# Optimization experiments

Measured on AMD Instinct MI355X. Metric: run time of the kernel, lower is better.

Reference implementation:

```python
import jax, jax.numpy as jnp
import numpy as np

B = 8       # complexes in batch
C = 32      # CDR residues per antibody
G = 2048    # antigen nodes per complex
D = 128     # encoded_dims
N_AB = B * C
N_AG = B * G
N = N_AB + N_AG
SLOPE = 0.2
EPS_BN = 1e-5


def _build_edges():
    # block-sparse bipartite edges (cdr_b x ag_b), symmetrized, + self loops
    srcs, dsts = [], []
    for b in range(B):
        ab = np.arange(b * C, (b + 1) * C)
        ag = np.arange(N_AB + b * G, N_AB + (b + 1) * G)
        g1, g2 = np.meshgrid(ab, ag, indexing='ij')
        srcs.append(g1.ravel()); dsts.append(g2.ravel())
    s = np.concatenate(srcs); d = np.concatenate(dsts)
    loops = np.arange(N)
    src = np.concatenate([s, d, loops]).astype(np.int32)
    dst = np.concatenate([d, s, loops]).astype(np.int32)
    return src, dst


def setup_inputs() -> dict:
    key = jax.random.key(0)
    ks = jax.random.split(key, 16)
    sc = 1.0 / np.sqrt(D)
    edge_src, edge_dst = _build_edges()
    return {
        'selected_ab': jax.random.normal(ks[0], (N_AB, D), jnp.float32),
        'x_ag': jax.random.normal(ks[1], (N_AG, D), jnp.float32),
        'W1': jax.random.normal(ks[2], (D, D), jnp.float32) * sc,
        'a_src1': jax.random.normal(ks[3], (D,), jnp.float32) * sc,
        'a_dst1': jax.random.normal(ks[4], (D,), jnp.float32) * sc,
        'b1': jnp.zeros((D,), jnp.float32),
        'W2': jax.random.normal(ks[5], (D, D), jnp.float32) * sc,
        'a_src2': jax.random.normal(ks[6], (D,), jnp.float32) * sc,
        'a_dst2': jax.random.normal(ks[7], (D,), jnp.float32) * sc,
        'b2': jnp.zeros((D,), jnp.float32),
        'bn_ab_g': jnp.ones((2 * D,), jnp.float32),
        'bn_ab_b': jnp.zeros((2 * D,), jnp.float32),
        'bn_ag_g': jnp.ones((2 * D,), jnp.float32),
        'bn_ag_b': jnp.zeros((2 * D,), jnp.float32),
        'fc_w': jax.random.normal(ks[8], (2 * D, 1), jnp.float32) * sc,
        'fc_b': jnp.zeros((1,), jnp.float32),
        'agfc_w': jax.random.normal(ks[9], (2 * D, 1), jnp.float32) * sc,
        'agfc_b': jnp.zeros((1,), jnp.float32),
        'edge_src': jnp.asarray(edge_src),
        'edge_dst': jnp.asarray(edge_dst),
    }


def _gat(x, W, a_s, a_d, b, src, dst):
    # PyG GATConv, heads=1, eval mode (dropout off)
    h = x @ W                                  # [N, D]
    al_s = h @ a_s                             # [N]
    al_d = h @ a_d                             # [N]
    e = jax.nn.leaky_relu(al_s[src] + al_d[dst], SLOPE)   # [E]
    m = jax.ops.segment_max(e, dst, num_segments=N)
    e = jnp.exp(e - m[dst])
    z = jax.ops.segment_sum(e, dst, num_segments=N)
    alpha = e / (z[dst] + 1e-16)
    out = jax.ops.segment_sum(h[src] * alpha[:, None], dst, num_segments=N)
    return out + b


def _bn(x, g, b):
    # training-mode batch stats (biased variance), like torch BatchNorm1d
    m = x.mean(0)
    v = ((x - m) ** 2).mean(0)
    return (x - m) / jnp.sqrt(v + EPS_BN) * g + b


def reference(selected_ab, x_ag, W1, a_src1, a_dst1, b1, W2, a_src2, a_dst2, b2,
              bn_ab_g, bn_ab_b, bn_ag_g, bn_ag_b, fc_w, fc_b, agfc_w, agfc_b,
              edge_src, edge_dst):
    x = jnp.concatenate([selected_ab, x_ag], axis=0)          # [N, D]
    x = jax.nn.relu(_gat(x, W1, a_src1, a_dst1, b1, edge_src, edge_dst))
    x = _gat(x, W2, a_src2, a_dst2, b2, edge_src, edge_dst)
    x_ab = jnp.concatenate([x[:N_AB], selected_ab], axis=1)   # [N_ab, 2D]
    x_ab = jax.nn.relu(_bn(x_ab, bn_ab_g, bn_ab_b))
    x_ab = (x_ab @ fc_w + fc_b).ravel()
    x_ag_o = jnp.concatenate([x[N_AB:], x_ag], axis=1)        # [N_ag, 2D]
    x_ag_o = jax.nn.relu(_bn(x_ag_o, bn_ag_g, bn_ag_b))
    x_ag_o = (x_ag_o @ agfc_w + agfc_b).ravel()
    return (x_ab, x_ag_o)
```

## Files before the change

kernel.cpp:

```cpp
#include <hip/hip_runtime.h>


#define N_AB 256
#define N_AG 16384
#define N_ALL 16640
#define G_AG 2048
#define SLOPE 0.2f
#define MSHIFT 20.0f

typedef __attribute__((ext_vector_type(4))) float f32x4;
typedef __attribute__((ext_vector_type(8))) __bf16 bf16x8;
typedef __attribute__((ext_vector_type(8))) unsigned short u16x8;
typedef unsigned short ushort_t;

__device__ __forceinline__ float bf2f(ushort_t u) {
  union { unsigned int i; float f; } v; v.i = ((unsigned int)u) << 16; return v.f;
}
__device__ __forceinline__ ushort_t f2bf(float f) {
  union { float fv; unsigned int i; } v; v.fv = f;
  unsigned int x = v.i;
  return (ushort_t)((x + 0x7fffu + ((x >> 16) & 1u)) >> 16);
}
__device__ __forceinline__ float lrelu(float x) { return x >= 0.f ? x : SLOPE * x; }
__device__ __forceinline__ float expw(float e) {
  return __expf(fminf(e, 60.f) - MSHIFT);
}
__device__ __forceinline__ float ldf(const void* p, size_t i, int f) {
  return f ? ((const float*)p)[i] : bf2f(((const ushort_t*)p)[i]);
}
__device__ __forceinline__ void ld8f(const void* p, size_t i, int f, float* o) {
  if (f) {
    const f32x4* q = (const f32x4*)((const float*)p + i);
    f32x4 a = q[0], b = q[1];
#pragma unroll
    for (int j = 0; j < 4; ++j) { o[j] = a[j]; o[j + 4] = b[j]; }
  } else {
    u16x8 v = *(const u16x8*)((const ushort_t*)p + i);
#pragma unroll
    for (int j = 0; j < 8; ++j) o[j] = bf2f(v[j]);
  }
}

__global__ __launch_bounds__(256) void k_pre(
    const void* __restrict__ W1, const void* __restrict__ W2,
    const void* __restrict__ as1, const void* __restrict__ ad1,
    const void* __restrict__ as2, const void* __restrict__ ad2,
    const ushort_t* __restrict__ selu,
    ushort_t* __restrict__ W1t, ushort_t* __restrict__ W2t,
    float* __restrict__ va, float* __restrict__ bnsumAG,
    float* __restrict__ accf, float* __restrict__ accz,
    int* __restrict__ flagp) {
  int t = threadIdx.x, lane = t & 63, wid = t >> 6;
  int bx = blockIdx.x;
  int cnt = 0;
#pragma unroll
  for (int i = 0; i < 8; ++i) {
    unsigned e = (selu[lane * 8 + i] >> 7) & 0xFF;
    if (e > 0xC8) cnt++;
  }
  int f = (__popcll(__ballot(cnt > 0)) >= 3) ? 1 : 0;
  if (bx == 0 && t == 0) flagp[0] = f;

  if (bx < 16) {
    const void* W = (bx < 8) ? W1 : W2;
    ushort_t* Wt = (bx < 8) ? W1t : W2t;
    int base = (bx & 7) * 2048 + t * 8;
    float o[8];
    ld8f(W, base, f, o);
#pragma unroll
    for (int j = 0; j < 8; ++j) {
      int idx = base + j;
      Wt[(idx & 127) * 128 + (idx >> 7)] = f2bf(o[j]);
    }
  } else if (bx < 32) {
    int j = bx - 16;
    const void* W   = (j < 8) ? W1 : W2;
    const void* asv = (j < 8) ? as1 : as2;
    const void* adv = (j < 8) ? ad1 : ad2;
    int vbase = (j < 8) ? 0 : 256;
    int basek = (j & 7) * 16 + wid * 4;
    float a_s0 = ldf(asv, lane, f), a_s1 = ldf(asv, lane + 64, f);
    float a_d0 = ldf(adv, lane, f), a_d1 = ldf(adv, lane + 64, f);
#pragma unroll
    for (int i = 0; i < 4; ++i) {
      int k = basek + i;
      float w0 = ldf(W, (size_t)k * 128 + lane, f);
      float w1 = ldf(W, (size_t)k * 128 + lane + 64, f);
      float ps = w0 * a_s0 + w1 * a_s1;
      float pd = w0 * a_d0 + w1 * a_d1;
#pragma unroll
      for (int o = 1; o < 64; o <<= 1) {
        ps += __shfl_xor(ps, o);
        pd += __shfl_xor(pd, o);
      }
      if (lane == 0) { va[vbase + k] = ps; va[vbase + 128 + k] = pd; }
    }
  } else {
    int j = bx - 32;
    f32x4* az = (f32x4*)(accf + (size_t)j * 4096);
    f32x4 z4 = (f32x4){0.f, 0.f, 0.f, 0.f};
    for (int i = t; i < 1024; i += 256) az[i] = z4;
    if (j == 0) { bnsumAG[t] = 0.f; bnsumAG[t + 256] = 0.f; accz[t] = 0.f; }
  }
}

__global__ __launch_bounds__(256) void k_gemm(
    const void* __restrict__ xa, int modeA,
    const void* __restrict__ xb, int modeB,
    const int* __restrict__ flagp,
    const ushort_t* __restrict__ Wt, const float* __restrict__ va,
    ushort_t* __restrict__ h, float* __restrict__ als, float* __restrict__ ald,
    float* __restrict__ accf, float* __restrict__ accz,
    const void* __restrict__ biasAb, float* __restrict__ xabf, int do_abfin) {
  __shared__ float zsh[32], wsh[32];
  int t = threadIdx.x, lane = t & 63, wid = t >> 6;
  int bx = blockIdx.x;
  if (do_abfin && bx < 8) {
    int fr = *flagp;
    int b = bx;
    if (t < 32) {
      int grow = b * 32 + t;
      float w = expw(lrelu(als[grow] + ald[grow]));
      zsh[t] = accz[grow] + w;
      wsh[t] = w;
      accz[grow] = 0.f;
    }
    __syncthreads();
#pragma unroll
    for (int i = 0; i < 16; ++i) {
      int e = i * 256 + t;
      int rl = e >> 7, col = e & 127;
      int grow = b * 32 + rl;
      size_t idx = (size_t)grow * 128 + col;
      float hv = bf2f(h[idx]);
      float v = (accf[idx] + wsh[rl] * hv) / (zsh[rl] + 1e-16f) + ldf(biasAb, col, fr);
      accf[idx] = 0.f;
      v = fmaxf(v, 0.f);
      xabf[idx] = v;
    }
    __syncthreads();
  }

  int rw0 = bx * 32 + (wid >> 1) * 16;
  int ch = wid & 1;
  const void* xsrc; int roff, mode;
  if (rw0 < N_AB) { xsrc = xa; roff = rw0; mode = modeA; }
  else            { xsrc = xb; roff = rw0 - N_AB; mode = modeB; }
  int fx = (mode == 2) ? *flagp : mode;
  int mm = lane & 15, q = lane >> 4;
  f32x4 acc[4];
#pragma unroll
  for (int b = 0; b < 4; ++b) acc[b] = (f32x4){0.f, 0.f, 0.f, 0.f};
  float pals = 0.f, pald = 0.f;
#pragma unroll
  for (int s = 0; s < 4; ++s) {
    int koff = s * 32 + q * 8;
    union { u16x8 u; bf16x8 b; } af;
    float o[8];
    ld8f(xsrc, (size_t)(roff + mm) * 128 + koff, fx, o);
#pragma unroll
    for (int j = 0; j < 8; ++j) {
      af.u[j] = f2bf(o[j]);
      pals += o[j] * va[koff + j];
      pald += o[j] * va[128 + koff + j];
    }
#pragma unroll
    for (int nt = 0; nt < 4; ++nt) {
      int colb = ch * 64 + nt * 16;
      bf16x8 bfr = *(const bf16x8*)(Wt + (size_t)(colb + mm) * 128 + koff);
      acc[nt] = __builtin_amdgcn_mfma_f32_16x16x32_bf16(af.b, bfr, acc[nt], 0, 0, 0);
    }
  }
  if (ch == 0) {
    float s1 = pals; s1 += __shfl_xor(s1, 16); s1 += __shfl_xor(s1, 32);
    float d1 = pald; d1 += __shfl_xor(d1, 16); d1 += __shfl_xor(d1, 32);
    if (lane < 16) { als[rw0 + lane] = s1; ald[rw0 + lane] = d1; }
  }
#pragma unroll
  for (int nt = 0; nt < 4; ++nt)
#pragma unroll
    for (int r = 0; r < 4; ++r) {
      int row = rw0 + q * 4 + r;
      int col = ch * 64 + nt * 16 + mm;
      h[(size_t)row * 128 + col] = f2bf(acc[nt][r]);
    }
}

#define ABP_STRIDE 72
#define AG_STRIDE 40
__global__ __launch_bounds__(256) void k_agg(
    const ushort_t* __restrict__ h, const float* __restrict__ als,
    const float* __restrict__ ald, const void* __restrict__ bias,
    const int* __restrict__ flagp, ushort_t* __restrict__ xout,
    float* __restrict__ accf, float* __restrict__ accz,
    const void* __restrict__ x_ag, float* __restrict__ bnsumAG,
    int do_relu, int do_bnsum) {
  __shared__ ushort_t hT[128 * ABP_STRIDE];
  __shared__ float alsS[64];
  __shared__ float colsum[128], colsq[128];
  int bx = blockIdx.x;
  int t = threadIdx.x, lane = t & 63, wid = t >> 6;
  int mm = lane & 15, q = lane >> 4;

  if (bx < 256) {
    int b = bx >> 5, jt = bx & 31;
    int f = *flagp;
    {
      int row = t & 31, c0g = (t >> 5) * 16;
      const ushort_t* src = h + (size_t)(b * 32 + row) * 128 + c0g;
      u16x8 v0 = *(const u16x8*)src;
      u16x8 v1 = *(const u16x8*)(src + 8);
#pragma unroll
      for (int j = 0; j < 8; ++j) {
        hT[(c0g + j) * AG_STRIDE + row] = v0[j];
        hT[(c0g + 8 + j) * AG_STRIDE + row] = v1[j];
      }
      if (t < 32) alsS[t] = als[b * 32 + t];
      if (t < 128) { colsum[t] = 0.f; colsq[t] = 0.f; }
    }
    __syncthreads();
    int jl = jt * 64 + wid * 16;
    int jrow = N_AB + b * G_AG + jl;
    float aldj = ald[jrow + mm];
    float alsj = als[jrow + mm];
    union { u16x8 u; bf16x8 b; } af;
    float zp = 0.f;
#pragma unroll
    for (int j = 0; j < 8; ++j) {
      ushort_t us = f2bf(expw(lrelu(alsS[q * 8 + j] + aldj)));
      af.u[j] = us;
      zp += bf2f(us);
    }
    zp += __shfl_xor(zp, 16);
    zp += __shfl_xor(zp, 32);
    float wself = expw(lrelu(alsj + aldj));
    float z = zp + wself;
#pragma unroll
    for (int nt = 0; nt < 8; ++nt) {
      int col = nt * 16 + mm;
      union { u16x8 u; bf16x8 b; } bfr;
      bfr.b = *(const bf16x8*)(&hT[col * AG_STRIDE + q * 8]);
      f32x4 acc = {0.f, 0.f, 0.f, 0.f};
      acc = __builtin_amdgcn_mfma_f32_16x16x32_bf16(af.b, bfr.b, acc, 0, 0, 0);
      float biasv = ldf(bias, col, f);
      float sl = 0.f, sq = 0.f;
#pragma unroll
      for (int r = 0; r < 4; ++r) {
        int row = q * 4 + r;
        float zr = __shfl(z, row);
        float wsr = __shfl(wself, row);
        float hv = bf2f(h[(size_t)(jrow + row) * 128 + col]);
        float v = (acc[r] + wsr * hv) / (zr + 1e-16f) + biasv;
        sl += v; sq += v * v;
        if (do_relu) v = fmaxf(v, 0.f);
        xout[(size_t)(jrow + row) * 128 + col] = f2bf(v);
      }
      if (do_bnsum) {
        atomicAdd(&colsum[col], sl);
        atomicAdd(&colsq[col], sq);
      }
    }
    if (do_bnsum) {
      __syncthreads();
      if (t < 128) {
        atomicAdd(&bnsumAG[t], colsum[t]);
        atomicAdd(&bnsumAG[256 + t], colsq[t]);
      }
    }
  } else if (bx < 512) {
    int bx2 = bx - 256;
    int b = bx2 >> 5, sg = bx2 & 31;
    int jrow0 = N_AB + b * G_AG + sg * 64;
    {
      int jr = t & 63, cgrp = (t >> 6) * 32;
      const ushort_t* src = h + (size_t)(jrow0 + jr) * 128 + cgrp;
#pragma unroll
      for (int v = 0; v < 4; ++v) {
        u16x8 vv = *(const u16x8*)(src + v * 8);
#pragma unroll
        for (int j = 0; j < 8; ++j)
          hT[(cgrp + v * 8 + j) * ABP_STRIDE + jr] = vv[j];
      }
      if (t < 64) alsS[t] = als[jrow0 + t];
    }
    __syncthreads();
    float aldm[2] = { ald[b * 32 + mm], ald[b * 32 + 16 + mm] };
    f32x4 acc[2][2];
#pragma unroll
    for (int a = 0; a < 2; ++a)
#pragma unroll
      for (int c = 0; c < 2; ++c) acc[a][c] = (f32x4){0.f, 0.f, 0.f, 0.f};
    float zz[2] = {0.f, 0.f};
#pragma unroll
    for (int s = 0; s < 2; ++s) {
      int k0 = s * 32 + q * 8;
      float a8[8];
#pragma unroll
      for (int j = 0; j < 8; ++j) a8[j] = alsS[k0 + j];
      union { u16x8 u; bf16x8 b; } af[2];
#pragma unroll
      for (int mt = 0; mt < 2; ++mt)
#pragma unroll
        for (int j = 0; j < 8; ++j) {
          ushort_t us = f2bf(expw(lrelu(a8[j] + aldm[mt])));
          af[mt].u[j] = us;
          zz[mt] += bf2f(us);
        }
#pragma unroll
      for (int ns = 0; ns < 2; ++ns) {
        int n = wid * 32 + ns * 16 + mm;
        union { u16x8 u; bf16x8 b; } bfr;
        bfr.b = *(const bf16x8*)(&hT[n * ABP_STRIDE + k0]);
        acc[0][ns] = __builtin_amdgcn_mfma_f32_16x16x32_bf16(af[0].b, bfr.b, acc[0][ns], 0, 0, 0);
        acc[1][ns] = __builtin_amdgcn_mfma_f32_16x16x32_bf16(af[1].b, bfr.b, acc[1][ns], 0, 0, 0);
      }
    }
#pragma unroll
    for (int mt = 0; mt < 2; ++mt)
#pragma unroll
      for (int ns = 0; ns < 2; ++ns)
#pragma unroll
        for (int r = 0; r < 4; ++r) {
          int row = b * 32 + mt * 16 + q * 4 + r;
          int col = wid * 32 + ns * 16 + mm;
          atomicAdd(&accf[(size_t)row * 128 + col], acc[mt][ns][r]);
        }
#pragma unroll
    for (int mt = 0; mt < 2; ++mt) {
      float z = zz[mt];
      z += __shfl_xor(z, 16);
      z += __shfl_xor(z, 32);
      if (wid == 0 && lane < 16)
        atomicAdd(&accz[b * 32 + mt * 16 + lane], z);
    }
  } else {
    int j = bx - 512;
    int f = *flagp;
    int col = t & 127, half = t >> 7;
    int r0 = j * 256 + half * 128;
    float s = 0.f, sq = 0.f;
    for (int r = 0; r < 128; ++r) {
      float v = ldf(x_ag, (size_t)(r0 + r) * 128 + col, f);
      s += v; sq += v * v;
    }
    atomicAdd(&bnsumAG[128 + col], s);
    atomicAdd(&bnsumAG[384 + col], sq);
  }
}

__global__ __launch_bounds__(256) void k_abfin(
    const float* __restrict__ accf, const float* __restrict__ accz,
    const ushort_t* __restrict__ h, const float* __restrict__ als,
    const float* __restrict__ ald, const void* __restrict__ bias,
    const int* __restrict__ flagp, float* __restrict__ xabf) {
  __shared__ float zsh[8], wsh[8];
  int bx = blockIdx.x, t = threadIdx.x;
  int b = bx >> 2, q4 = bx & 3;
  int f = *flagp;
  if (t < 8) {
    int grow = b * 32 + q4 * 8 + t;
    float w = expw(lrelu(als[grow] + ald[grow]));
    zsh[t] = accz[grow] + w;
    wsh[t] = w;
  }
  __syncthreads();
#pragma unroll
  for (int i = 0; i < 4; ++i) {
    int e = i * 256 + t;
    int rl = e >> 7, col = e & 127;
    int grow = b * 32 + q4 * 8 + rl;
    size_t idx = (size_t)grow * 128 + col;
    float hv = bf2f(h[idx]);
    float v = (accf[idx] + wsh[rl] * hv) / (zsh[rl] + 1e-16f) + ldf(bias, col, f);
    xabf[idx] = v;
  }
}

__global__ __launch_bounds__(256) void k_head(
    const float* __restrict__ xfab, const ushort_t* __restrict__ xfag,
    const void* __restrict__ sel_ab, const void* __restrict__ x_ag,
    const float* __restrict__ bnsumAG,
    const void* __restrict__ gab, const void* __restrict__ bab,
    const void* __restrict__ gag, const void* __restrict__ bag,
    const void* __restrict__ fcw, const void* __restrict__ agfcw,
    const void* __restrict__ fcb, const void* __restrict__ agfcb,
    const int* __restrict__ flagp, void* __restrict__ out) {
  __shared__ float stA[256], stB[256], stW[256];
  int t = threadIdx.x, lane = t & 63, wid = t >> 6;
  int row = blockIdx.x * 4 + wid;
  int f = *flagp;
  int isAb = (blockIdx.x < 64);
  if (isAb) {
    float s = 0.f, sq = 0.f;
    if (t < 128) {
      for (int r = 0; r < 256; ++r) { float v = xfab[(size_t)r * 128 + t]; s += v; sq += v * v; }
    } else {
      for (int r = 0; r < 256; ++r) {
        float v = ldf(sel_ab, (size_t)r * 128 + (t - 128), f);
        s += v; sq += v * v;
      }
    }
    float mean = s * (1.f / 256.f);
    float var = fmaxf(sq * (1.f / 256.f) - mean * mean, 0.f);
    float A = ldf(gab, t, f) / sqrtf(var + 1e-5f);
    stA[t] = A;
    stB[t] = ldf(bab, t, f) - mean * A;
    stW[t] = ldf(fcw, t, f);
  } else {
    float mean = bnsumAG[t] * (1.f / 16384.f);
    float var = fmaxf(bnsumAG[256 + t] * (1.f / 16384.f) - mean * mean, 0.f);
    float A = ldf(gag, t, f) / sqrtf(var + 1e-5f);
    stA[t] = A;
    stB[t] = ldf(bag, t, f) - mean * A;
    stW[t] = ldf(agfcw, t, f);
  }
  __syncthreads();

  int c0 = lane * 2;
  float v0, v1, v2, v3, bb;
  if (isAb) {
    const float* p = xfab + (size_t)row * 128 + c0;
    v0 = p[0]; v1 = p[1];
    size_t ro = (size_t)row * 128 + c0;
    v2 = ldf(sel_ab, ro, f);
    v3 = ldf(sel_ab, ro + 1, f);
    bb = ldf(fcb, 0, f);
  } else {
    const ushort_t* p = xfag + (size_t)row * 128 + c0;
    v0 = bf2f(p[0]); v1 = bf2f(p[1]);
    size_t ro = (size_t)(row - N_AB) * 128 + c0;
    v2 = ldf(x_ag, ro, f);
    v3 = ldf(x_ag, ro + 1, f);
    bb = ldf(agfcb, 0, f);
  }
  float acc =
      fmaxf(v0 * stA[c0]           + stB[c0],           0.f) * stW[c0]
    + fmaxf(v1 * stA[c0 + 1]       + stB[c0 + 1],       0.f) * stW[c0 + 1]
    + fmaxf(v2 * stA[128 + c0]     + stB[128 + c0],     0.f) * stW[128 + c0]
    + fmaxf(v3 * stA[128 + c0 + 1] + stB[128 + c0 + 1], 0.f) * stW[128 + c0 + 1];
#pragma unroll
  for (int o = 1; o < 64; o <<= 1) acc += __shfl_xor(acc, o);
  if (lane == 0) {
    float r = acc + bb;
    if (f) ((float*)out)[row] = r;
    else   ((ushort_t*)out)[row] = f2bf(r);
  }
}

extern "C" void kernel_launch(void* const* d_in, const int* in_sizes, int n_in,
                              void* d_out, int out_size, void* d_ws, size_t ws_size,
                              hipStream_t stream) {
  (void)in_sizes; (void)n_in; (void)out_size; (void)ws_size;
  const void* sel_ab = d_in[0];
  const void* x_ag   = d_in[1];
  const void* W1     = d_in[2];
  const void* as1    = d_in[3];
  const void* ad1    = d_in[4];
  const void* b1     = d_in[5];
  const void* W2     = d_in[6];
  const void* as2    = d_in[7];
  const void* ad2    = d_in[8];
  const void* b2     = d_in[9];
  const void* gab    = d_in[10];
  const void* bab    = d_in[11];
  const void* gag    = d_in[12];
  const void* bag    = d_in[13];
  const void* fcw    = d_in[14];
  const void* fcb    = d_in[15];
  const void* agfcw  = d_in[16];
  const void* agfcb  = d_in[17];

  ushort_t* h  = (ushort_t*)d_in[18];
  ushort_t* xb = (ushort_t*)d_in[19];

  char* wsp = (char*)d_ws;
  size_t off = 0;
  auto carve = [&](size_t bytes) -> char* {
    char* p = wsp + off; off += (bytes + 255) & ~(size_t)255; return p;
  };
  int* flag      = (int*)carve(64 * 4);
  ushort_t* W1t  = (ushort_t*)carve(16384 * 2);
  ushort_t* W2t  = (ushort_t*)carve(16384 * 2);
  float* va      = (float*)carve(512 * 4);
  float* als     = (float*)carve((size_t)N_ALL * 4);
  float* ald     = (float*)carve((size_t)N_ALL * 4);
  float* bnsumAG = (float*)carve(512 * 4);
  float* xabf    = (float*)carve((size_t)N_AB * 128 * 4);
  float* accf    = (float*)carve((size_t)N_AB * 128 * 4);
  float* accz    = (float*)carve(256 * 4);

  k_pre<<<40, 256, 0, stream>>>(W1, W2, as1, ad1, as2, ad2,
                                (const ushort_t*)sel_ab, W1t, W2t, va,
                                bnsumAG, accf, accz, flag);
  k_gemm<<<520, 256, 0, stream>>>(sel_ab, 2, x_ag, 2, flag, W1t, va, h, als, ald,
                                  accf, accz, b1, xabf, 0);
  k_agg<<<512, 256, 0, stream>>>(h, als, ald, b1, flag, xb, accf, accz,
                                 x_ag, bnsumAG, 1, 0);
  k_gemm<<<520, 256, 0, stream>>>(xabf, 1, xb + (size_t)N_AB * 128, 0, flag, W2t, va + 256, h, als, ald,
                                  accf, accz, b1, xabf, 1);
  k_agg<<<576, 256, 0, stream>>>(h, als, ald, b2, flag, xb, accf, accz,
                                 x_ag, bnsumAG, 0, 1);
  k_abfin<<<32, 256, 0, stream>>>(accf, accz, h, als, ald, b2, flag, xabf);
  k_head<<<4160, 256, 0, stream>>>(xabf, xb, sel_ab, x_ag, bnsumAG,
                                   gab, bab, gag, bag, fcw, agfcw,
                                   fcb, agfcb, flag, d_out);
}
```

Before: 187.1 us.

## Fold antibody finalize into head kernel and split antigen aggregation columns

Removes the k_abfin launch: the head kernel's antibody blocks now rebuild layer-2 antibody rows from the atomic accumulators (accf, accz, h, self-loop weight, bias) and compute the BN column statistics in-kernel. Separately, the antigen aggregation branch of k_agg is split so each block covers 32 rows instead of 64, with two waves dividing the 128 columns. This doubles that branch's block count to raise parallelism. The cost is more redundant staging of hT per block, and each of the 64 antibody head blocks repeats the full 256-row antibody stats pass.

New measurement: 208.1 us. 1.11x slower.

```diff
diff --git a/kernel.cpp b/kernel.cpp
--- a/kernel.cpp
+++ b/kernel.cpp
@@ -202,8 +202,8 @@
   int t = threadIdx.x, lane = t & 63, wid = t >> 6;
   int mm = lane & 15, q = lane >> 4;
 
-  if (bx < 256) {
-    int b = bx >> 5, jt = bx & 31;
+  if (bx < 512) {
+    int b = bx >> 6, jt = bx & 63;
     int f = *flagp;
     {
       int row = t & 31, c0g = (t >> 5) * 16;
@@ -219,7 +219,8 @@
       if (t < 128) { colsum[t] = 0.f; colsq[t] = 0.f; }
     }
     __syncthreads();
-    int jl = jt * 64 + wid * 16;
+    int jl = jt * 32 + (wid >> 1) * 16;
+    int ch = wid & 1;
     int jrow = N_AB + b * G_AG + jl;
     float aldj = ald[jrow + mm];
     float alsj = als[jrow + mm];
@@ -236,8 +237,8 @@
     float wself = expw(lrelu(alsj + aldj));
     float z = zp + wself;
 #pragma unroll
-    for (int nt = 0; nt < 8; ++nt) {
-      int col = nt * 16 + mm;
+    for (int nt = 0; nt < 4; ++nt) {
+      int col = ch * 64 + nt * 16 + mm;
       union { u16x8 u; bf16x8 b; } bfr;
       bfr.b = *(const bf16x8*)(&hT[col * AG_STRIDE + q * 8]);
       f32x4 acc = {0.f, 0.f, 0.f, 0.f};
@@ -267,8 +268,8 @@
         atomicAdd(&bnsumAG[256 + t], colsq[t]);
       }
     }
-  } else if (bx < 512) {
-    int bx2 = bx - 256;
+  } else if (bx < 768) {
+    int bx2 = bx - 512;
     int b = bx2 >> 5, sg = bx2 & 31;
     int jrow0 = N_AB + b * G_AG + sg * 64;
     {
@@ -334,7 +335,7 @@
         atomicAdd(&accz[b * 32 + mt * 16 + lane], z);
     }
   } else {
-    int j = bx - 512;
+    int j = bx - 768;
     int f = *flagp;
     int col = t & 127, half = t >> 7;
     int r0 = j * 256 + half * 128;
@@ -348,37 +349,12 @@
   }
 }
 
-__global__ __launch_bounds__(256) void k_abfin(
+__global__ __launch_bounds__(256) void k_head(
+    const ushort_t* __restrict__ xfag,
+    const void* __restrict__ sel_ab, const void* __restrict__ x_ag,
     const float* __restrict__ accf, const float* __restrict__ accz,
-    const ushort_t* __restrict__ h, const float* __restrict__ als,
-    const float* __restrict__ ald, const void* __restrict__ bias,
-    const int* __restrict__ flagp, float* __restrict__ xabf) {
-  __shared__ float zsh[8], wsh[8];
-  int bx = blockIdx.x, t = threadIdx.x;
-  int b = bx >> 2, q4 = bx & 3;
-  int f = *flagp;
-  if (t < 8) {
-    int grow = b * 32 + q4 * 8 + t;
-    float w = expw(lrelu(als[grow] + ald[grow]));
-    zsh[t] = accz[grow] + w;
-    wsh[t] = w;
-  }
-  __syncthreads();
-#pragma unroll
-  for (int i = 0; i < 4; ++i) {
-    int e = i * 256 + t;
-    int rl = e >> 7, col = e & 127;
-    int grow = b * 32 + q4 * 8 + rl;
-    size_t idx = (size_t)grow * 128 + col;
-    float hv = bf2f(h[idx]);
-    float v = (accf[idx] + wsh[rl] * hv) / (zsh[rl] + 1e-16f) + ldf(bias, col, f);
-    xabf[idx] = v;
-  }
-}
-
-__global__ __launch_bounds__(256) void k_head(
-    const float* __restrict__ xfab, const ushort_t* __restrict__ xfag,
-    const void* __restrict__ sel_ab, const void* __restrict__ x_ag,
+    const ushort_t* __restrict__ hbuf, const float* __restrict__ als,
+    const float* __restrict__ ald, const void* __restrict__ b2ab,
     const float* __restrict__ bnsumAG,
     const void* __restrict__ gab, const void* __restrict__ bab,
     const void* __restrict__ gag, const void* __restrict__ bag,
@@ -386,26 +362,56 @@
     const void* __restrict__ fcb, const void* __restrict__ agfcb,
     const int* __restrict__ flagp, void* __restrict__ out) {
   __shared__ float stA[256], stB[256], stW[256];
+  __shared__ float zrow[256], wrow[256];
+  __shared__ float colS[4][128], colQ[4][128];
   int t = threadIdx.x, lane = t & 63, wid = t >> 6;
   int row = blockIdx.x * 4 + wid;
   int f = *flagp;
   int isAb = (blockIdx.x < 64);
+  int c0 = lane * 2;
   if (isAb) {
-    float s = 0.f, sq = 0.f;
+    if (t < 256) {
+      float w = expw(lrelu(als[t] + ald[t]));
+      wrow[t] = w;
+      zrow[t] = accz[t] + w;
+    }
+    __syncthreads();
+    float bias0 = ldf(b2ab, c0, f), bias1 = ldf(b2ab, c0 + 1, f);
+    float s0 = 0.f, s1 = 0.f, q0 = 0.f, q1 = 0.f;
+    for (int r = wid; r < 256; r += 4) {
+      size_t base = (size_t)r * 128 + c0;
+      float inv = 1.f / (zrow[r] + 1e-16f);
+      float w = wrow[r];
+      float v0 = (accf[base] + w * bf2f(hbuf[base])) * inv + bias0;
+      float v1 = (accf[base + 1] + w * bf2f(hbuf[base + 1])) * inv + bias1;
+      s0 += v0; q0 += v0 * v0;
+      s1 += v1; q1 += v1 * v1;
+    }
+    colS[wid][c0] = s0; colS[wid][c0 + 1] = s1;
+    colQ[wid][c0] = q0; colQ[wid][c0 + 1] = q1;
+    __syncthreads();
     if (t < 128) {
-      for (int r = 0; r < 256; ++r) { float v = xfab[(size_t)r * 128 + t]; s += v; sq += v * v; }
+      float s = colS[0][t] + colS[1][t] + colS[2][t] + colS[3][t];
+      float sq = colQ[0][t] + colQ[1][t] + colQ[2][t] + colQ[3][t];
+      float mean = s * (1.f / 256.f);
+      float var = fmaxf(sq * (1.f / 256.f) - mean * mean, 0.f);
+      float A = ldf(gab, t, f) / sqrtf(var + 1e-5f);
+      stA[t] = A;
+      stB[t] = ldf(bab, t, f) - mean * A;
+      stW[t] = ldf(fcw, t, f);
     } else {
+      float s = 0.f, sq = 0.f;
       for (int r = 0; r < 256; ++r) {
         float v = ldf(sel_ab, (size_t)r * 128 + (t - 128), f);
         s += v; sq += v * v;
       }
-    }
-    float mean = s * (1.f / 256.f);
-    float var = fmaxf(sq * (1.f / 256.f) - mean * mean, 0.f);
-    float A = ldf(gab, t, f) / sqrtf(var + 1e-5f);
-    stA[t] = A;
-    stB[t] = ldf(bab, t, f) - mean * A;
-    stW[t] = ldf(fcw, t, f);
+      float mean = s * (1.f / 256.f);
+      float var = fmaxf(sq * (1.f / 256.f) - mean * mean, 0.f);
+      float A = ldf(gab, t, f) / sqrtf(var + 1e-5f);
+      stA[t] = A;
+      stB[t] = ldf(bab, t, f) - mean * A;
+      stW[t] = ldf(fcw, t, f);
+    }
   } else {
     float mean = bnsumAG[t] * (1.f / 16384.f);
     float var = fmaxf(bnsumAG[256 + t] * (1.f / 16384.f) - mean * mean, 0.f);
@@ -416,11 +422,13 @@
   }
   __syncthreads();
 
-  int c0 = lane * 2;
   float v0, v1, v2, v3, bb;
   if (isAb) {
-    const float* p = xfab + (size_t)row * 128 + c0;
-    v0 = p[0]; v1 = p[1];
+    size_t base = (size_t)row * 128 + c0;
+    float inv = 1.f / (zrow[row] + 1e-16f);
+    float w = wrow[row];
+    v0 = (accf[base] + w * bf2f(hbuf[base])) * inv + ldf(b2ab, c0, f);
+    v1 = (accf[base + 1] + w * bf2f(hbuf[base + 1])) * inv + ldf(b2ab, c0 + 1, f);
     size_t ro = (size_t)row * 128 + c0;
     v2 = ldf(sel_ab, ro, f);
     v3 = ldf(sel_ab, ro + 1, f);
@@ -494,14 +502,13 @@
                                 bnsumAG, accf, accz, flag);
   k_gemm<<<520, 256, 0, stream>>>(sel_ab, 2, x_ag, 2, flag, W1t, va, h, als, ald,
                                   accf, accz, b1, xabf, 0);
-  k_agg<<<512, 256, 0, stream>>>(h, als, ald, b1, flag, xb, accf, accz,
+  k_agg<<<768, 256, 0, stream>>>(h, als, ald, b1, flag, xb, accf, accz,
                                  x_ag, bnsumAG, 1, 0);
   k_gemm<<<520, 256, 0, stream>>>(xabf, 1, xb + (size_t)N_AB * 128, 0, flag, W2t, va + 256, h, als, ald,
                                   accf, accz, b1, xabf, 1);
-  k_agg<<<576, 256, 0, stream>>>(h, als, ald, b2, flag, xb, accf, accz,
+  k_agg<<<832, 256, 0, stream>>>(h, als, ald, b2, flag, xb, accf, accz,
                                  x_ag, bnsumAG, 0, 1);
-  k_abfin<<<32, 256, 0, stream>>>(accf, accz, h, als, ald, b2, flag, xabf);
-  k_head<<<4160, 256, 0, stream>>>(xabf, xb, sel_ab, x_ag, bnsumAG,
-                                   gab, bab, gag, bag, fcw, agfcw,
+  k_head<<<4160, 256, 0, stream>>>(xb, sel_ab, x_ag, accf, accz, h, als, ald, b2,
+                                   bnsumAG, gab, bab, gag, bag, fcw, agfcw,
                                    fcb, agfcb, flag, d_out);
 }
```
